# Optimization experiments

Hardware: AMD Instinct MI355X
Metric: run time of the kernel (lower is better)

The kernel has to match this reference:

```python
import jax, jax.numpy as jnp
import numpy as np

B, F, P, DM = 1, 16, 256, 1024            # batch, frames, patches, mm_hidden_size
HID = 4096                                 # config.hidden_size
DI, DSTATE, DTRANK, DCONV = 2 * DM, 16, DM // 16, 4


def _layernorm(x, w, b):
    mu = x.mean(-1, keepdims=True)
    var = ((x - mu) ** 2).mean(-1, keepdims=True)
    return (x - mu) * jax.lax.rsqrt(var + 1e-5) * w + b


def _selective_scan(u, dt, A, Bm, Cm, Dv):
    # u, dt: [b,L,d]; Bm, Cm: [b,L,n]; A: [d,n]; Dv: [d]
    def step(h, inp):
        dt_t, B_t, C_t, u_t = inp  # [b,d],[b,n],[b,n],[b,d]
        h = jnp.exp(dt_t[..., None] * A) * h + (dt_t * u_t)[..., None] * B_t[:, None, :]
        return h, jnp.einsum('bdn,bn->bd', h, C_t)
    h0 = jnp.zeros((u.shape[0], A.shape[0], A.shape[1]), u.dtype)
    _, ys = jax.lax.scan(step, h0, (jnp.swapaxes(dt, 0, 1), jnp.swapaxes(Bm, 0, 1),
                                    jnp.swapaxes(Cm, 0, 1), jnp.swapaxes(u, 0, 1)))
    return jnp.swapaxes(ys, 0, 1) + u * Dv


def _mamba_block(x, ln_w, ln_b, in_proj_w, conv_w, conv_b, x_proj_w,
                 dt_proj_w, dt_proj_b, A_log, D_param, out_proj_w):
    res = x
    x = _layernorm(x, ln_w, ln_b)
    xz = x @ in_proj_w                       # [b,L,2*DI]
    xin, z = jnp.split(xz, 2, axis=-1)
    xt = jnp.swapaxes(xin, 1, 2)             # [b,DI,L]
    xt = jax.lax.conv_general_dilated(xt, conv_w[:, None, :], (1,), [(DCONV - 1, 0)],
                                      dimension_numbers=('NCH', 'OIH', 'NCH'),
                                      feature_group_count=DI)
    xt = xt + conv_b[:, None]
    u = jax.nn.silu(jnp.swapaxes(xt, 1, 2))  # [b,L,DI]
    x_dbl = u @ x_proj_w                     # [b,L,DTRANK+2*DSTATE]
    dt_raw, Bm, Cm = jnp.split(x_dbl, [DTRANK, DTRANK + DSTATE], axis=-1)
    dt = jax.nn.softplus(dt_raw @ dt_proj_w + dt_proj_b)
    A = -jnp.exp(A_log)
    y = _selective_scan(u, dt, A, Bm, Cm, D_param)
    y = y * jax.nn.silu(z)
    return res + y @ out_proj_w


def setup_inputs() -> dict:
    key = jax.random.key(0)
    ks = jax.random.split(key, 8)
    s = 0.02
    return {
        'vst': jax.random.normal(ks[0], (B, F, P, DM), jnp.float32),
        'ln_w': jnp.ones((DM,), jnp.float32), 'ln_b': jnp.zeros((DM,), jnp.float32),
        'in_proj_w': jax.random.normal(ks[1], (DM, 2 * DI), jnp.float32) * s,
        'conv_w': jax.random.normal(ks[2], (DI, DCONV), jnp.float32) * s,
        'conv_b': jnp.zeros((DI,), jnp.float32),
        'x_proj_w': jax.random.normal(ks[3], (DI, DTRANK + 2 * DSTATE), jnp.float32) * s,
        'dt_proj_w': jax.random.normal(ks[4], (DTRANK, DI), jnp.float32) * s,
        'dt_proj_b': jnp.full((DI,), -4.6, jnp.float32),  # softplus ~ 0.01
        'A_log': jnp.log(jnp.tile(jnp.arange(1, DSTATE + 1, dtype=jnp.float32), (DI, 1))),
        'D_param': jnp.ones((DI,), jnp.float32),
        'out_proj_w': jax.random.normal(ks[5], (DI, DM), jnp.float32) * s,
        'fln_w': jnp.ones((DM,), jnp.float32), 'fln_b': jnp.zeros((DM,), jnp.float32),
        'mlp_w1': jax.random.normal(ks[6], (DM, HID), jnp.float32) * s,
        'mlp_b1': jnp.zeros((HID,), jnp.float32),
        'mlp_w2': jax.random.normal(ks[7], (HID, HID), jnp.float32) * s,
        'mlp_b2': jnp.zeros((HID,), jnp.float32),
    }


def reference(vst, ln_w, ln_b, in_proj_w, conv_w, conv_b, x_proj_w, dt_proj_w,
              dt_proj_b, A_log, D_param, out_proj_w, fln_w, fln_b,
              mlp_w1, mlp_b1, mlp_w2, mlp_b2):
    b, f, p, d = vst.shape
    h = w = int(p ** 0.5)
    # the chain of rearranges in the source is a net reshape to b (f h w) d
    x = vst.reshape(b, f * h * w, d)
    x = _mamba_block(x, ln_w, ln_b, in_proj_w, conv_w, conv_b, x_proj_w,
                     dt_proj_w, dt_proj_b, A_log, D_param, out_proj_w)
    x = _layernorm(x, fln_w, fln_b)
    # AvgPool3d kernel=(1,4,4), stride=(1,4,4) over (f,h,w)
    x = x.reshape(b, f, h // 4, 4, w // 4, 4, d).mean(axis=(3, 5))
    x = x.reshape(b, f * (h // 4) * (w // 4), d)
    y = jax.nn.gelu(x @ mlp_w1 + mlp_b1, approximate=False)
    return y @ mlp_w2 + mlp_b2
```

## Files before the change

### kernel.cpp

```cpp
#include <hip/hip_runtime.h>
#include <hip/hip_bf16.h>
#include <math.h>

typedef __hip_bfloat16 bf16_t;
typedef __attribute__((ext_vector_type(8))) short short8;
typedef __attribute__((ext_vector_type(4))) float f32x4;

#define L_SEQ   4096
#define DMODEL  1024
#define DI      2048
#define NST     16
#define DTRANK  64
#define XDBL_N  96
#define HID     4096
#define CHUNK   32
#define NCHUNK  128
#define POOLED_ROWS 256

__device__ __forceinline__ void async_load16(const bf16_t* g, bf16_t* l) {
    __builtin_amdgcn_global_load_lds(
        (const __attribute__((address_space(1))) void*)g,
        (__attribute__((address_space(3))) void*)l,
        16, 0, 0);
}
__device__ __forceinline__ void async_load16f(const float* g, float* l) {
    __builtin_amdgcn_global_load_lds(
        (const __attribute__((address_space(1))) void*)g,
        (__attribute__((address_space(3))) void*)l,
        16, 0, 0);
}

__device__ __forceinline__ float softplus_f(float x) {
    return fmaxf(x, 0.f) + __logf(1.f + __expf(-fabsf(x)));
}

__global__ __launch_bounds__(256)
void transpose_all_kernel(const float* __restrict__ j0, bf16_t* __restrict__ o0,
                          const float* __restrict__ j1, bf16_t* __restrict__ o1,
                          const float* __restrict__ j2, bf16_t* __restrict__ o2,
                          const float* __restrict__ j3, bf16_t* __restrict__ o3,
                          const float* __restrict__ j4, bf16_t* __restrict__ o4) {
    int b = blockIdx.x;
    const float* in; bf16_t* out; int K, N, Npad, local;
    if (b < 512)        { in = j0; out = o0; K = 1024; N = 4096; Npad = 4096; local = b; }
    else if (b < 544)   { in = j1; out = o1; K = 2048; N = 96;   Npad = 128;  local = b - 512; }
    else if (b < 576)   { in = j2; out = o2; K = 64;   N = 2048; Npad = 2048; local = b - 544; }
    else if (b < 832)   { in = j3; out = o3; K = 2048; N = 1024; Npad = 1024; local = b - 576; }
    else                { in = j4; out = o4; K = 1024; N = 4096; Npad = 4096; local = b - 832; }
    int nt = Npad >> 6;
    int k0 = (local / nt) << 7, n0 = (local % nt) << 6;

    __shared__ float t[64 * 129];
    int tid = threadIdx.x;
    int kkb = tid >> 4;
    int nq  = (tid & 15) * 4;
#pragma unroll
    for (int it = 0; it < 8; it++) {
        int kl = it * 16 + kkb;
        int gk = k0 + kl, gn = n0 + nq;
        float4 v = {0.f, 0.f, 0.f, 0.f};
        if (gk < K) {
            const float* src = in + (size_t)gk * N + gn;
            if (gn + 3 < N) v = *(const float4*)src;
            else {
                if (gn + 0 < N) v.x = src[0];
                if (gn + 1 < N) v.y = src[1];
                if (gn + 2 < N) v.z = src[2];
                if (gn + 3 < N) v.w = src[3];
            }
        }
        t[(nq + 0) * 129 + kl] = v.x;
        t[(nq + 1) * 129 + kl] = v.y;
        t[(nq + 2) * 129 + kl] = v.z;
        t[(nq + 3) * 129 + kl] = v.w;
    }
    __syncthreads();
#pragma unroll
    for (int it = 0; it < 4; it++) {
        int slot = it * 256 + tid;
        int nn = slot >> 4, kc = (slot & 15) * 8;
        if (k0 + kc >= K) continue;
        const float* r = &t[nn * 129 + kc];
        short8 o;
#pragma unroll
        for (int j = 0; j < 8; j++) {
            bf16_t h = __float2bfloat16(r[j]);
            o[j] = *(short*)&h;
        }
        *(short8*)(out + (size_t)(n0 + nn) * K + k0 + kc) = o;
    }
}

__global__ __launch_bounds__(256)
void ln_kernel(const float* __restrict__ x, const float* __restrict__ w,
               const float* __restrict__ b, bf16_t* __restrict__ out) {
    int row = blockIdx.x;
    int tid = threadIdx.x;
    const float* xr = x + (size_t)row * DMODEL;
    float v[4];
    float s = 0.f, ss = 0.f;
#pragma unroll
    for (int e = 0; e < 4; e++) {
        v[e] = xr[tid + e * 256];
        s += v[e];
        ss += v[e] * v[e];
    }
#pragma unroll
    for (int off = 32; off > 0; off >>= 1) {
        s  += __shfl_down(s, off);
        ss += __shfl_down(ss, off);
    }
    __shared__ float rs[4], rss[4];
    int wid = tid >> 6;
    if ((tid & 63) == 0) { rs[wid] = s; rss[wid] = ss; }
    __syncthreads();
    s  = rs[0] + rs[1] + rs[2] + rs[3];
    ss = rss[0] + rss[1] + rss[2] + rss[3];
    float mu  = s * (1.f / DMODEL);
    float var = ss * (1.f / DMODEL) - mu * mu;
    float inv = rsqrtf(var + 1e-5f);
#pragma unroll
    for (int e = 0; e < 4; e++) {
        int col = tid + e * 256;
        out[(size_t)row * DMODEL + col] =
            __float2bfloat16((v[e] - mu) * inv * w[col] + b[col]);
    }
}

__global__ __launch_bounds__(256)
void ln_pool2_kernel(const bf16_t* __restrict__ part, size_t pstride,
                     const float* __restrict__ res, const float* __restrict__ w,
                     const float* __restrict__ b, bf16_t* __restrict__ pooled) {
    int p = blockIdx.x;
    int tid = threadIdx.x;
    int f = p >> 4, i4 = (p >> 2) & 3, j4 = p & 3;
    __shared__ float rs[4], rss[4];
    float acc[4] = {0.f, 0.f, 0.f, 0.f};
    float wv[4], bv[4];
#pragma unroll
    for (int e = 0; e < 4; e++) { wv[e] = w[tid + e * 256]; bv[e] = b[tid + e * 256]; }
    for (int r16 = 0; r16 < 16; r16++) {
        int ii = r16 >> 2, jj = r16 & 3;
        int row = f * 256 + (i4 * 4 + ii) * 16 + j4 * 4 + jj;
        size_t ro = (size_t)row * DMODEL;
        float v[4];
        float s = 0.f, ss = 0.f;
#pragma unroll
        for (int e = 0; e < 4; e++) {
            int col = tid + e * 256;
            float x = res[ro + col]
                    + __bfloat162float(part[ro + col])
                    + __bfloat162float(part[pstride + ro + col]);
            v[e] = x;
            s += x;
            ss += x * x;
        }
#pragma unroll
        for (int off = 32; off > 0; off >>= 1) {
            s  += __shfl_down(s, off);
            ss += __shfl_down(ss, off);
        }
        int wid = tid >> 6;
        if ((tid & 63) == 0) { rs[wid] = s; rss[wid] = ss; }
        __syncthreads();
        s  = rs[0] + rs[1] + rs[2] + rs[3];
        ss = rss[0] + rss[1] + rss[2] + rss[3];
        float mu  = s * (1.f / DMODEL);
        float var = ss * (1.f / DMODEL) - mu * mu;
        float inv = rsqrtf(var + 1e-5f);
#pragma unroll
        for (int e = 0; e < 4; e++)
            acc[e] += (v[e] - mu) * inv * wv[e] + bv[e];
        __syncthreads();
    }
#pragma unroll
    for (int e = 0; e < 4; e++)
        pooled[(size_t)p * DMODEL + tid + e * 256] = __float2bfloat16(acc[e] * (1.f / 16.f));
}

template <int EPI>
__global__ __launch_bounds__(256, 2)
void mfma_gemm(const bf16_t* __restrict__ A, int lda,
               const bf16_t* __restrict__ Bt, int ldb,
               int K,
               float* __restrict__ Cf, bf16_t* __restrict__ Cb, int ldc,
               const float* __restrict__ bias, const float* __restrict__ res) {
    __shared__ bf16_t Asl[128 * 32];
    __shared__ bf16_t Bsl[128 * 32];
    const int tid = threadIdx.x;
    const int l = tid & 63, w = tid >> 6;
    const int m0 = blockIdx.y * 128, n0 = blockIdx.x * 128;
    const int wm = (w >> 1) * 64, wn = (w & 1) * 64;

    const int srow = tid >> 2;
    const int skc = (tid & 3) * 8;
    const bf16_t* Ag = A + (size_t)(m0 + srow) * lda + skc;
    const bf16_t* Bg = Bt + (size_t)(n0 + srow) * ldb + skc;
    bf16_t* As0 = Asl + (size_t)(w * 64) * 8;
    bf16_t* As1 = Asl + (size_t)(256 + w * 64) * 8;
    bf16_t* Bs0 = Bsl + (size_t)(w * 64) * 8;
    bf16_t* Bs1 = Bsl + (size_t)(256 + w * 64) * 8;

    f32x4 acc[4][4];
#pragma unroll
    for (int i = 0; i < 4; i++)
#pragma unroll
        for (int j = 0; j < 4; j++) acc[i][j] = (f32x4){0.f, 0.f, 0.f, 0.f};

    const short8* Asv = (const short8*)Asl;
    const short8* Bsv = (const short8*)Bsl;
    const int fr = l >> 4;
    const int fc = l & 15;

    for (int k0 = 0; k0 < K; k0 += 32) {
        __syncthreads();
        async_load16(Ag, As0);
        async_load16(Ag + (size_t)64 * lda, As1);
        async_load16(Bg, Bs0);
        async_load16(Bg + (size_t)64 * ldb, Bs1);
        Ag += 32; Bg += 32;
        __syncthreads();

        short8 a[4], b[4];
#pragma unroll
        for (int im = 0; im < 4; im++)
            a[im] = Asv[(wm + im * 16 + fc) * 4 + fr];
#pragma unroll
        for (int in = 0; in < 4; in++)
            b[in] = Bsv[(wn + in * 16 + fc) * 4 + fr];
#pragma unroll
        for (int im = 0; im < 4; im++)
#pragma unroll
            for (int in = 0; in < 4; in++)
                acc[im][in] = __builtin_amdgcn_mfma_f32_16x16x32_bf16(
                    a[im], b[in], acc[im][in], 0, 0, 0);
    }

#pragma unroll
    for (int im = 0; im < 4; im++) {
        int mbase = m0 + wm + im * 16 + fr * 4;
#pragma unroll
        for (int in = 0; in < 4; in++) {
            int n = n0 + wn + in * 16 + fc;
            float bv = (EPI == 1) ? bias[n] : 0.f;
#pragma unroll
            for (int v = 0; v < 4; v++) {
                float x = acc[im][in][v];
                size_t off = (size_t)(mbase + v) * ldc + n;
                if (EPI == 0) {
                    Cb[off] = __float2bfloat16(x);
                } else if (EPI == 1) {
                    Cb[off] = __float2bfloat16(softplus_f(x + bv));
                }
            }
        }
    }
}

template <bool PBF16>
__global__ __launch_bounds__(256, 2)
void mfma_gemm_splitk(const bf16_t* __restrict__ A, int lda,
                      const bf16_t* __restrict__ Bt, int ldb,
                      int Kper, void* __restrict__ Cpart, int ldc,
                      size_t pstride) {
    __shared__ bf16_t Asl[128 * 32];
    __shared__ bf16_t Bsl[128 * 32];
    const int tid = threadIdx.x;
    const int l = tid & 63, w = tid >> 6;
    const int m0 = blockIdx.y * 128, n0 = blockIdx.x * 128;
    const int wm = (w >> 1) * 64, wn = (w & 1) * 64;
    const int kbase = blockIdx.z * Kper;

    const int srow = tid >> 2;
    const int skc = (tid & 3) * 8;
    const bf16_t* Ag = A + (size_t)(m0 + srow) * lda + kbase + skc;
    const bf16_t* Bg = Bt + (size_t)(n0 + srow) * ldb + kbase + skc;
    bf16_t* As0 = Asl + (size_t)(w * 64) * 8;
    bf16_t* As1 = Asl + (size_t)(256 + w * 64) * 8;
    bf16_t* Bs0 = Bsl + (size_t)(w * 64) * 8;
    bf16_t* Bs1 = Bsl + (size_t)(256 + w * 64) * 8;

    f32x4 acc[4][4];
#pragma unroll
    for (int i = 0; i < 4; i++)
#pragma unroll
        for (int j = 0; j < 4; j++) acc[i][j] = (f32x4){0.f, 0.f, 0.f, 0.f};

    const short8* Asv = (const short8*)Asl;
    const short8* Bsv = (const short8*)Bsl;
    const int fr = l >> 4;
    const int fc = l & 15;

    for (int k0 = 0; k0 < Kper; k0 += 32) {
        __syncthreads();
        async_load16(Ag, As0);
        async_load16(Ag + (size_t)64 * lda, As1);
        async_load16(Bg, Bs0);
        async_load16(Bg + (size_t)64 * ldb, Bs1);
        Ag += 32; Bg += 32;
        __syncthreads();

        short8 a[4], b[4];
#pragma unroll
        for (int im = 0; im < 4; im++)
            a[im] = Asv[(wm + im * 16 + fc) * 4 + fr];
#pragma unroll
        for (int in = 0; in < 4; in++)
            b[in] = Bsv[(wn + in * 16 + fc) * 4 + fr];
#pragma unroll
        for (int im = 0; im < 4; im++)
#pragma unroll
            for (int in = 0; in < 4; in++)
                acc[im][in] = __builtin_amdgcn_mfma_f32_16x16x32_bf16(
                    a[im], b[in], acc[im][in], 0, 0, 0);
    }

#pragma unroll
    for (int im = 0; im < 4; im++) {
        int mbase = m0 + wm + im * 16 + fr * 4;
#pragma unroll
        for (int in = 0; in < 4; in++) {
            int n = n0 + wn + in * 16 + fc;
#pragma unroll
            for (int v = 0; v < 4; v++) {
                size_t o = (size_t)(mbase + v) * ldc + n;
                if (PBF16)
                    ((bf16_t*)Cpart)[(size_t)blockIdx.z * pstride + o] =
                        __float2bfloat16(acc[im][in][v]);
                else
                    ((float*)Cpart)[(size_t)blockIdx.z * pstride + o] = acc[im][in][v];
            }
        }
    }
}

__global__ __launch_bounds__(512, 1)
void gemm_nt_kernel(const bf16_t* __restrict__ A, int lda,
                    const float* __restrict__ B, int ldb,
                    int Kper, float* __restrict__ Cpart, int ldc,
                    size_t pstride) {
    __shared__ bf16_t Asl[256 * 32];
    __shared__ float  Bsl[32 * 64];
    const int tid = threadIdx.x;
    const int l = tid & 63, w = tid >> 6;
    const int n0 = blockIdx.x * 64;
    const int kbase = blockIdx.z * Kper;
    const int wm = w * 32;

    const int a_row = tid >> 2, a_kc = (tid & 3) * 8;
    const bf16_t* Ag = A + (size_t)a_row * lda + kbase + a_kc;
    bf16_t* As0 = Asl + (size_t)(w * 64) * 8;
    bf16_t* As1 = Asl + (size_t)(512 + w * 64) * 8;
    const int b_row = tid >> 4, b_nc = (tid & 15) * 4;
    const float* Bg = B + (size_t)(kbase + b_row) * ldb + n0 + b_nc;
    float* Bs0 = Bsl + (size_t)(w * 64) * 4;

    f32x4 acc[2][4];
#pragma unroll
    for (int i = 0; i < 2; i++)
#pragma unroll
        for (int j = 0; j < 4; j++) acc[i][j] = (f32x4){0.f, 0.f, 0.f, 0.f};

    const short8* Asv = (const short8*)Asl;
    const int fr = l >> 4, fc = l & 15;

    for (int k0 = 0; k0 < Kper; k0 += 32) {
        __syncthreads();
        async_load16(Ag, As0);
        async_load16(Ag + (size_t)128 * lda, As1);
        async_load16f(Bg, Bs0);
        Ag += 32;
        Bg += (size_t)32 * ldb;
        __syncthreads();

        short8 a[2], bfr[4];
        a[0] = Asv[(wm + fc) * 4 + fr];
        a[1] = Asv[(wm + 16 + fc) * 4 + fr];
#pragma unroll
        for (int j = 0; j < 4; j++) {
            const float* bp = Bsl + (size_t)(fr * 8) * 64 + j * 16 + fc;
            short8 t;
#pragma unroll
            for (int i = 0; i < 8; i++) {
                bf16_t h = __float2bfloat16(bp[i * 64]);
                t[i] = *(short*)&h;
            }
            bfr[j] = t;
        }
#pragma unroll
        for (int im = 0; im < 2; im++)
#pragma unroll
            for (int j = 0; j < 4; j++)
                acc[im][j] = __builtin_amdgcn_mfma_f32_16x16x32_bf16(
                    a[im], bfr[j], acc[im][j], 0, 0, 0);
    }

    float* Cz = Cpart + (size_t)blockIdx.z * pstride;
#pragma unroll
    for (int im = 0; im < 2; im++) {
        int mbase = wm + im * 16 + fr * 4;
#pragma unroll
        for (int j = 0; j < 4; j++) {
            int n = n0 + j * 16 + fc;
#pragma unroll
            for (int v = 0; v < 4; v++)
                Cz[(size_t)(mbase + v) * ldc + n] = acc[im][j][v];
        }
    }
}

template <int S, int EPI>
__global__ __launch_bounds__(256)
void reduce_splitk(const float* __restrict__ part, size_t pstride, int ldp,
                   int M, int N, float* __restrict__ outf, bf16_t* __restrict__ outb,
                   int ldo, const float* __restrict__ bias) {
    int idx = blockIdx.x * 256 + threadIdx.x;
    if (idx >= M * N) return;
    int r = idx / N, c = idx - r * N;
    float s = 0.f;
#pragma unroll
    for (int z = 0; z < S; z++)
        s += part[(size_t)z * pstride + (size_t)r * ldp + c];
    size_t o = (size_t)r * ldo + c;
    if (EPI == 0) {
        outf[o] = s;
        outb[o] = __float2bfloat16(s);
    } else if (EPI == 1) {
        s += bias[c];
        s = 0.5f * s * (1.f + erff(s * 0.70710678118654752f));
        outb[o] = __float2bfloat16(s);
    } else {
        outf[o] = s + bias[c];
    }
}

__global__ __launch_bounds__(256)
void conv_silu_kernel(const bf16_t* __restrict__ xz, const float* __restrict__ cw,
                      const float* __restrict__ cb, bf16_t* __restrict__ u) {
    int idx = blockIdx.x * 256 + threadIdx.x;
    if (idx >= L_SEQ * DI / 2) return;
    int chp = idx & (DI / 2 - 1);
    int l   = idx >> 10;
    int ch  = chp * 2;
    float acc0 = cb[ch], acc1 = cb[ch + 1];
    const float4* cwv = (const float4*)(cw + ch * 4);
    float4 c0 = cwv[0], c1 = cwv[1];
    float w0[4] = {c0.x, c0.y, c0.z, c0.w};
    float w1[4] = {c1.x, c1.y, c1.z, c1.w};
#pragma unroll
    for (int k = 0; k < 4; k++) {
        int ls = l - 3 + k;
        if (ls >= 0) {
            const bf16_t* p = xz + (size_t)ls * (2 * DI) + ch;
            acc0 += w0[k] * __bfloat162float(p[0]);
            acc1 += w1[k] * __bfloat162float(p[1]);
        }
    }
    float s0 = acc0 / (1.f + __expf(-acc0));
    float s1 = acc1 / (1.f + __expf(-acc1));
    bf16_t o0 = __float2bfloat16(s0), o1 = __float2bfloat16(s1);
    unsigned int packed = (unsigned int)*(unsigned short*)&o0 |
                          ((unsigned int)*(unsigned short*)&o1 << 16);
    *(unsigned int*)(u + (size_t)l * DI + ch) = packed;
}

__global__ __launch_bounds__(256)
void scan_pass1(const bf16_t* __restrict__ dt, const bf16_t* __restrict__ u,
                const float* __restrict__ x_dbl, const float* __restrict__ A_log,
                float* __restrict__ dtsum, float* __restrict__ Sw) {
    int c = blockIdx.x;
    int tid = threadIdx.x;
    int lane = tid & 63, w = tid >> 6;
    int dloc = w * 32 + (lane & 31);
    int n0 = (lane >> 5) * 8;
    int d = blockIdx.y * 128 + dloc;
    int l0 = c * CHUNK;
    __shared__ float sB[CHUNK * NST];
    for (int i = tid; i < CHUNK * NST; i += 256)
        sB[i] = x_dbl[(size_t)(l0 + (i >> 4)) * XDBL_N + DTRANK + (i & 15)];
    __syncthreads();
    float Areg[8], h[8];
#pragma unroll
    for (int j = 0; j < 8; j++) {
        Areg[j] = -__expf(A_log[d * NST + n0 + j]);
        h[j] = 0.f;
    }
    float dts = 0.f;
    float dtl = __bfloat162float(dt[(size_t)l0 * DI + d]);
    float ul  = __bfloat162float(u[(size_t)l0 * DI + d]);
    for (int l = 0; l < CHUNK; l++) {
        float dtn = 0.f, un = 0.f;
        if (l + 1 < CHUNK) {
            int gl = l0 + l + 1;
            dtn = __bfloat162float(dt[(size_t)gl * DI + d]);
            un  = __bfloat162float(u[(size_t)gl * DI + d]);
        }
        float du = dtl * ul;
        dts += dtl;
#pragma unroll
        for (int j = 0; j < 8; j++) {
            float a = __expf(dtl * Areg[j]);
            h[j] = a * h[j] + du * sB[l * NST + n0 + j];
        }
        dtl = dtn; ul = un;
    }
    size_t base = ((size_t)c * DI + d) * NST + n0;
#pragma unroll
    for (int j = 0; j < 8; j++)
        Sw[base + j] = h[j];
    if (n0 == 0)
        dtsum[(size_t)c * DI + d] = dts;
}

__global__ __launch_bounds__(256)
void scan_pass2(const float* __restrict__ dtsum, const float* __restrict__ A_log,
                float* __restrict__ SwInit) {
    int tid = blockIdx.x * 256 + threadIdx.x;
    if (tid >= DI * NST) return;
    int d = tid >> 4;
    float A = -__expf(A_log[tid]);
    const int DN = DI * NST;
    size_t idx = tid;
    float h = 0.f;
    float ds = dtsum[d], s = SwInit[idx];
    for (int c = 0; c < NCHUNK; c++) {
        size_t nidx = idx + DN;
        float dsn = 0.f, sn = 0.f;
        if (c + 1 < NCHUNK) {
            dsn = dtsum[(size_t)(c + 1) * DI + d];
            sn  = SwInit[nidx];
        }
        float p = __expf(ds * A);
        SwInit[idx] = h;
        h = p * h + s;
        ds = dsn; s = sn; idx = nidx;
    }
}

__global__ __launch_bounds__(256)
void scan_pass3(const bf16_t* __restrict__ dt, const bf16_t* __restrict__ u,
                const float* __restrict__ x_dbl, const float* __restrict__ A_log,
                const float* __restrict__ Dp, const float* __restrict__ initw,
                const bf16_t* __restrict__ xz, bf16_t* __restrict__ yy) {
    int c = blockIdx.x;
    int tid = threadIdx.x;
    int lane = tid & 63, w = tid >> 6;
    int dloc = w * 32 + (lane & 31);
    int n0 = (lane >> 5) * 8;
    int d = blockIdx.y * 128 + dloc;
    int l0 = c * CHUNK;
    __shared__ float sBC[CHUNK * 2 * NST];
    for (int i = tid; i < CHUNK * 2 * NST; i += 256)
        sBC[i] = x_dbl[(size_t)(l0 + (i >> 5)) * XDBL_N + DTRANK + (i & 31)];
    __syncthreads();
    float Areg[8], h[8];
    size_t base = ((size_t)c * DI + d) * NST + n0;
#pragma unroll
    for (int j = 0; j < 8; j++) {
        Areg[j] = -__expf(A_log[d * NST + n0 + j]);
        h[j] = initw[base + j];
    }
    float Dd = Dp[d];
    float dtl = __bfloat162float(dt[(size_t)l0 * DI + d]);
    float ul  = __bfloat162float(u[(size_t)l0 * DI + d]);
    float zv  = __bfloat162float(xz[(size_t)l0 * (2 * DI) + DI + d]);
    for (int l = 0; l < CHUNK; l++) {
        float dtn = 0.f, un = 0.f, zn = 0.f;
        if (l + 1 < CHUNK) {
            int gl = l0 + l + 1;
            dtn = __bfloat162float(dt[(size_t)gl * DI + d]);
            un  = __bfloat162float(u[(size_t)gl * DI + d]);
            zn  = __bfloat162float(xz[(size_t)gl * (2 * DI) + DI + d]);
        }
        float du = dtl * ul;
        float y = 0.f;
#pragma unroll
        for (int j = 0; j < 8; j++) {
            float a = __expf(dtl * Areg[j]);
            h[j] = a * h[j] + du * sBC[l * 32 + n0 + j];
            y += h[j] * sBC[l * 32 + NST + n0 + j];
        }
        y += __shfl_xor(y, 32);
        float sz = zv / (1.f + __expf(-zv));
        if ((lane >> 5) == 0)
            yy[(size_t)(l0 + l) * DI + d] = __float2bfloat16((y + ul * Dd) * sz);
        dtl = dtn; ul = un; zv = zn;
    }
}

extern "C" void kernel_launch(void* const* d_in, const int* in_sizes, int n_in,
                              void* d_out, int out_size, void* d_ws, size_t ws_size,
                              hipStream_t stream) {
    const float* vst        = (const float*)d_in[0];
    const float* ln_w       = (const float*)d_in[1];
    const float* ln_b       = (const float*)d_in[2];
    const float* in_proj_w  = (const float*)d_in[3];
    const float* conv_w     = (const float*)d_in[4];
    const float* conv_b     = (const float*)d_in[5];
    const float* x_proj_w   = (const float*)d_in[6];
    const float* dt_proj_w  = (const float*)d_in[7];
    const float* dt_proj_b  = (const float*)d_in[8];
    const float* A_log      = (const float*)d_in[9];
    const float* D_param    = (const float*)d_in[10];
    const float* out_proj_w = (const float*)d_in[11];
    const float* fln_w      = (const float*)d_in[12];
    const float* fln_b      = (const float*)d_in[13];
    const float* mlp_w1     = (const float*)d_in[14];
    const float* mlp_b1     = (const float*)d_in[15];
    const float* mlp_w2     = (const float*)d_in[16];
    const float* mlp_b2     = (const float*)d_in[17];
    float* out = (float*)d_out;

    char* wsb = (char*)d_ws;
    size_t off = 0;
    auto alloc_bf = [&](size_t n) { bf16_t* p = (bf16_t*)(wsb + off); off += n * 2; return p; };
    auto alloc_f  = [&](size_t n) { float*  p = (float*)(wsb + off); off += n * 4; return p; };

    bf16_t* w1t  = alloc_bf((size_t)(2 * DI) * DMODEL);
    bf16_t* xpt  = alloc_bf((size_t)128 * DI);
    bf16_t* dtpt = alloc_bf((size_t)DI * DTRANK);
    bf16_t* opt  = alloc_bf((size_t)DMODEL * DI);
    bf16_t* m1t  = alloc_bf((size_t)HID * DMODEL);
    bf16_t* m2t  = alloc_bf((size_t)HID * HID);
    bf16_t* xz_bf   = alloc_bf((size_t)L_SEQ * 2 * DI);
    bf16_t* u_bf    = alloc_bf((size_t)L_SEQ * DI);
    bf16_t* dt_bf   = alloc_bf((size_t)L_SEQ * DI);
    bf16_t* xdbl_bf = alloc_bf((size_t)L_SEQ * XDBL_N);
    bf16_t* yy_bf   = alloc_bf((size_t)L_SEQ * DI);
    float*  xdbl_f  = alloc_f((size_t)L_SEQ * XDBL_N);
    float*  Pw      = alloc_f((size_t)NCHUNK * DI * NST);
    float*  Sw      = alloc_f((size_t)NCHUNK * DI * NST);
    bf16_t* xn_bf   = yy_bf;
    float*  g2part  = Pw;
    float*  dtsum   = Pw;
    bf16_t* g4part  = xz_bf;
    bf16_t* pooled  = dt_bf;
    bf16_t* h1_bf   = dt_bf + (size_t)POOLED_ROWS * DMODEL;
    float*  g5part  = (float*)yy_bf;
    float*  g6part  = (float*)m2t;

    dim3 blk256(256);

    transpose_all_kernel<<<1344, blk256, 0, stream>>>(
        in_proj_w, w1t, x_proj_w, xpt, dt_proj_w, dtpt,
        out_proj_w, opt, mlp_w1, m1t);

    ln_kernel<<<L_SEQ, blk256, 0, stream>>>(vst, ln_w, ln_b, xn_bf);

    mfma_gemm<0><<<dim3((2 * DI) / 128, L_SEQ / 128), blk256, 0, stream>>>(
        xn_bf, DMODEL, w1t, DMODEL, DMODEL, nullptr, xz_bf, 2 * DI, nullptr, nullptr);

    conv_silu_kernel<<<(L_SEQ * DI / 2) / 256, blk256, 0, stream>>>(xz_bf, conv_w, conv_b, u_bf);

    mfma_gemm_splitk<false><<<dim3(1, L_SEQ / 128, 8), blk256, 0, stream>>>(
        u_bf, DI, xpt, DI, DI / 8, g2part, 128, (size_t)L_SEQ * 128);
    reduce_splitk<8, 0><<<(L_SEQ * XDBL_N) / 256, blk256, 0, stream>>>(
        g2part, (size_t)L_SEQ * 128, 128, L_SEQ, XDBL_N, xdbl_f, xdbl_bf, XDBL_N, nullptr);

    mfma_gemm<1><<<dim3(DI / 128, L_SEQ / 128), blk256, 0, stream>>>(
        xdbl_bf, XDBL_N, dtpt, DTRANK, DTRANK, nullptr, dt_bf, DI, dt_proj_b, nullptr);

    scan_pass1<<<dim3(NCHUNK, DI / 128), blk256, 0, stream>>>(
        dt_bf, u_bf, xdbl_f, A_log, dtsum, Sw);
    scan_pass2<<<(DI * NST) / 256, blk256, 0, stream>>>(dtsum, A_log, Sw);
    scan_pass3<<<dim3(NCHUNK, DI / 128), blk256, 0, stream>>>(
        dt_bf, u_bf, xdbl_f, A_log, D_param, Sw, xz_bf, yy_bf);

    mfma_gemm_splitk<true><<<dim3(DMODEL / 128, L_SEQ / 128, 2), blk256, 0, stream>>>(
        yy_bf, DI, opt, DI, DI / 2, g4part, DMODEL, (size_t)L_SEQ * DMODEL);

    ln_pool2_kernel<<<POOLED_ROWS, blk256, 0, stream>>>(
        g4part, (size_t)L_SEQ * DMODEL, vst, fln_w, fln_b, pooled);

    mfma_gemm_splitk<false><<<dim3(HID / 128, POOLED_ROWS / 128, 4), blk256, 0, stream>>>(
        pooled, DMODEL, m1t, DMODEL, DMODEL / 4, g5part, HID, (size_t)POOLED_ROWS * HID);
    reduce_splitk<4, 1><<<(POOLED_ROWS * HID) / 256, blk256, 0, stream>>>(
        g5part, (size_t)POOLED_ROWS * HID, HID, POOLED_ROWS, HID, nullptr, h1_bf, HID, mlp_b1);

    gemm_nt_kernel<<<dim3(HID / 64, 1, 8), dim3(512), 0, stream>>>(
        h1_bf, HID, mlp_w2, HID, HID / 8, g6part, HID, (size_t)POOLED_ROWS * HID);
    reduce_splitk<8, 2><<<(POOLED_ROWS * HID) / 256, blk256, 0, stream>>>(
        g6part, (size_t)POOLED_ROWS * HID, HID, POOLED_ROWS, HID, out, nullptr, HID, mlp_b2);
}
```

Before: 450.2 us.

## Split LN-pool across more blocks, vectorize split-K reductions, batch scan pass2 loads

The final layernorm+pool kernel is split into 1024 blocks, each handling 4 rows and writing fp32 partials, followed by a small kernel that sums the 4 partials per pooled row. This raises parallelism from 256 blocks. The split-K reduce kernels now process 4 columns per thread with vector loads and stores. scan_pass2 loads 8 chunks of inputs at a time to expose memory-level parallelism in its serial loop. The cost is an extra launch and an fp32 partial buffer round trip through yy_bf.

```diff
diff --git a/kernel.cpp b/kernel.cpp
--- a/kernel.cpp
+++ b/kernel.cpp
@@ -128,10 +128,11 @@
 }
 
 __global__ __launch_bounds__(256)
-void ln_pool2_kernel(const bf16_t* __restrict__ part, size_t pstride,
-                     const float* __restrict__ res, const float* __restrict__ w,
-                     const float* __restrict__ b, bf16_t* __restrict__ pooled) {
-    int p = blockIdx.x;
+void ln_pool_a_kernel(const bf16_t* __restrict__ part, size_t pstride,
+                      const float* __restrict__ res, const float* __restrict__ w,
+                      const float* __restrict__ b, float* __restrict__ pool_part) {
+    int blk = blockIdx.x;
+    int p = blk >> 2, ii = blk & 3;
     int tid = threadIdx.x;
     int f = p >> 4, i4 = (p >> 2) & 3, j4 = p & 3;
     __shared__ float rs[4], rss[4];
@@ -139,8 +140,7 @@
     float wv[4], bv[4];
 #pragma unroll
     for (int e = 0; e < 4; e++) { wv[e] = w[tid + e * 256]; bv[e] = b[tid + e * 256]; }
-    for (int r16 = 0; r16 < 16; r16++) {
-        int ii = r16 >> 2, jj = r16 & 3;
+    for (int jj = 0; jj < 4; jj++) {
         int row = f * 256 + (i4 * 4 + ii) * 16 + j4 * 4 + jj;
         size_t ro = (size_t)row * DMODEL;
         float v[4];
@@ -175,7 +175,19 @@
     }
 #pragma unroll
     for (int e = 0; e < 4; e++)
-        pooled[(size_t)p * DMODEL + tid + e * 256] = __float2bfloat16(acc[e] * (1.f / 16.f));
+        pool_part[(size_t)blk * DMODEL + tid + e * 256] = acc[e];
+}
+
+__global__ __launch_bounds__(256)
+void ln_pool_b_kernel(const float* __restrict__ pool_part, bf16_t* __restrict__ pooled) {
+    int idx = blockIdx.x * 256 + threadIdx.x;
+    if (idx >= POOLED_ROWS * DMODEL) return;
+    int p = idx >> 10, col = idx & (DMODEL - 1);
+    float s = pool_part[(size_t)(p * 4 + 0) * DMODEL + col]
+            + pool_part[(size_t)(p * 4 + 1) * DMODEL + col]
+            + pool_part[(size_t)(p * 4 + 2) * DMODEL + col]
+            + pool_part[(size_t)(p * 4 + 3) * DMODEL + col];
+    pooled[idx] = __float2bfloat16(s * (1.f / 16.f));
 }
 
 template <int EPI>
@@ -411,26 +423,43 @@
 
 template <int S, int EPI>
 __global__ __launch_bounds__(256)
-void reduce_splitk(const float* __restrict__ part, size_t pstride, int ldp,
-                   int M, int N, float* __restrict__ outf, bf16_t* __restrict__ outb,
-                   int ldo, const float* __restrict__ bias) {
+void reduce_splitk4(const float* __restrict__ part, size_t pstride, int ldp,
+                    int M, int N, float* __restrict__ outf, bf16_t* __restrict__ outb,
+                    int ldo, const float* __restrict__ bias) {
     int idx = blockIdx.x * 256 + threadIdx.x;
-    if (idx >= M * N) return;
-    int r = idx / N, c = idx - r * N;
-    float s = 0.f;
+    int npr = N >> 2;
+    if (idx >= M * npr) return;
+    int r = idx / npr, c = (idx - r * npr) << 2;
+    f32x4 s = (f32x4){0.f, 0.f, 0.f, 0.f};
 #pragma unroll
     for (int z = 0; z < S; z++)
-        s += part[(size_t)z * pstride + (size_t)r * ldp + c];
+        s += *(const f32x4*)(part + (size_t)z * pstride + (size_t)r * ldp + c);
     size_t o = (size_t)r * ldo + c;
     if (EPI == 0) {
-        outf[o] = s;
-        outb[o] = __float2bfloat16(s);
+        *(f32x4*)(outf + o) = s;
+        short8 pk;
+        ushort4 ub;
+#pragma unroll
+        for (int e = 0; e < 4; e++) {
+            bf16_t h = __float2bfloat16(s[e]);
+            ((unsigned short*)&ub)[e] = *(unsigned short*)&h;
+        }
+        *(ushort4*)(outb + o) = ub;
+        (void)pk;
     } else if (EPI == 1) {
-        s += bias[c];
-        s = 0.5f * s * (1.f + erff(s * 0.70710678118654752f));
-        outb[o] = __float2bfloat16(s);
+        f32x4 bv = *(const f32x4*)(bias + c);
+        ushort4 ub;
+#pragma unroll
+        for (int e = 0; e < 4; e++) {
+            float x = s[e] + bv[e];
+            x = 0.5f * x * (1.f + erff(x * 0.70710678118654752f));
+            bf16_t h = __float2bfloat16(x);
+            ((unsigned short*)&ub)[e] = *(unsigned short*)&h;
+        }
+        *(ushort4*)(outb + o) = ub;
     } else {
-        outf[o] = s + bias[c];
+        f32x4 bv = *(const f32x4*)(bias + c);
+        *(f32x4*)(outf + o) = s + bv;
     }
 }
 
@@ -519,21 +548,21 @@
     if (tid >= DI * NST) return;
     int d = tid >> 4;
     float A = -__expf(A_log[tid]);
-    const int DN = DI * NST;
-    size_t idx = tid;
+    const size_t DN = DI * NST;
     float h = 0.f;
-    float ds = dtsum[d], s = SwInit[idx];
-    for (int c = 0; c < NCHUNK; c++) {
-        size_t nidx = idx + DN;
-        float dsn = 0.f, sn = 0.f;
-        if (c + 1 < NCHUNK) {
-            dsn = dtsum[(size_t)(c + 1) * DI + d];
-            sn  = SwInit[nidx];
-        }
-        float p = __expf(ds * A);
-        SwInit[idx] = h;
-        h = p * h + s;
-        ds = dsn; s = sn; idx = nidx;
+    for (int c = 0; c < NCHUNK; c += 8) {
+        float ds8[8], s8[8];
+#pragma unroll
+        for (int j = 0; j < 8; j++) {
+            ds8[j] = dtsum[(size_t)(c + j) * DI + d];
+            s8[j]  = SwInit[(size_t)(c + j) * DN + tid];
+        }
+#pragma unroll
+        for (int j = 0; j < 8; j++) {
+            float p = __expf(ds8[j] * A);
+            SwInit[(size_t)(c + j) * DN + tid] = h;
+            h = p * h + s8[j];
+        }
     }
 }
 
@@ -636,6 +665,7 @@
     bf16_t* g4part  = xz_bf;
     bf16_t* pooled  = dt_bf;
     bf16_t* h1_bf   = dt_bf + (size_t)POOLED_ROWS * DMODEL;
+    float*  pool_part = (float*)yy_bf;
     float*  g5part  = (float*)yy_bf;
     float*  g6part  = (float*)m2t;
 
@@ -654,7 +684,7 @@
 
     mfma_gemm_splitk<false><<<dim3(1, L_SEQ / 128, 8), blk256, 0, stream>>>(
         u_bf, DI, xpt, DI, DI / 8, g2part, 128, (size_t)L_SEQ * 128);
-    reduce_splitk<8, 0><<<(L_SEQ * XDBL_N) / 256, blk256, 0, stream>>>(
+    reduce_splitk4<8, 0><<<(L_SEQ * (XDBL_N / 4) + 255) / 256, blk256, 0, stream>>>(
         g2part, (size_t)L_SEQ * 128, 128, L_SEQ, XDBL_N, xdbl_f, xdbl_bf, XDBL_N, nullptr);
 
     mfma_gemm<1><<<dim3(DI / 128, L_SEQ / 128), blk256, 0, stream>>>(
@@ -669,16 +699,18 @@
     mfma_gemm_splitk<true><<<dim3(DMODEL / 128, L_SEQ / 128, 2), blk256, 0, stream>>>(
         yy_bf, DI, opt, DI, DI / 2, g4part, DMODEL, (size_t)L_SEQ * DMODEL);
 
-    ln_pool2_kernel<<<POOLED_ROWS, blk256, 0, stream>>>(
-        g4part, (size_t)L_SEQ * DMODEL, vst, fln_w, fln_b, pooled);
+    ln_pool_a_kernel<<<1024, blk256, 0, stream>>>(
+        g4part, (size_t)L_SEQ * DMODEL, vst, fln_w, fln_b, pool_part);
+    ln_pool_b_kernel<<<(POOLED_ROWS * DMODEL) / 256, blk256, 0, stream>>>(
+        pool_part, pooled);
 
     mfma_gemm_splitk<false><<<dim3(HID / 128, POOLED_ROWS / 128, 4), blk256, 0, stream>>>(
         pooled, DMODEL, m1t, DMODEL, DMODEL / 4, g5part, HID, (size_t)POOLED_ROWS * HID);
-    reduce_splitk<4, 1><<<(POOLED_ROWS * HID) / 256, blk256, 0, stream>>>(
+    reduce_splitk4<4, 1><<<(POOLED_ROWS * (HID / 4)) / 256, blk256, 0, stream>>>(
         g5part, (size_t)POOLED_ROWS * HID, HID, POOLED_ROWS, HID, nullptr, h1_bf, HID, mlp_b1);
 
     gemm_nt_kernel<<<dim3(HID / 64, 1, 8), dim3(512), 0, stream>>>(
         h1_bf, HID, mlp_w2, HID, HID / 8, g6part, HID, (size_t)POOLED_ROWS * HID);
-    reduce_splitk<8, 2><<<(POOLED_ROWS * HID) / 256, blk256, 0, stream>>>(
+    reduce_splitk4<8, 2><<<(POOLED_ROWS * (HID / 4)) / 256, blk256, 0, stream>>>(
         g6part, (size_t)POOLED_ROWS * HID, HID, POOLED_ROWS, HID, out, nullptr, HID, mlp_b2);
 }
```

Measured after the change: 431.9 us. -4.1%, faster.
